# Optimization experiments

Measured on AMD Instinct MI355X. Metric: run time of the kernel, lower is better.

Reference implementation:

```python
import jax, jax.numpy as jnp
import numpy as np

H = 128  # hidden_dim
F = 256  # node_feature_dim
N = 40000      # layer-graph nodes
E = 640000     # layer-graph edges
L = 8          # number of head graphs
NH = 8192      # nodes per head graph
EH = 131072    # edges per head graph


def setup_inputs() -> dict:
    key = jax.random.key(0)
    ks = jax.random.split(key, 32)
    s = 0.05
    inp = {
        "x": jax.random.normal(ks[0], (N, F), jnp.float32),
        "edge_index": jax.random.randint(ks[1], (2, E), 0, N, jnp.int64) if jax.config.jax_enable_x64 else jax.random.randint(ks[1], (2, E), 0, N, jnp.int32),
        "head_x": jax.random.normal(ks[2], (L, NH, F), jnp.float32),
        "head_edge_index": jax.random.randint(ks[3], (L, 2, EH), 0, NH, jnp.int32),
        # feature encoder (Linear-ReLU-Linear-ReLU)
        "enc_w1": jax.random.normal(ks[4], (F, H), jnp.float32) * s, "enc_b1": jnp.zeros((H,), jnp.float32),
        "enc_w2": jax.random.normal(ks[5], (H, H), jnp.float32) * s, "enc_b2": jnp.zeros((H,), jnp.float32),
        # two GCNConv layers
        "gnn_w1": jax.random.normal(ks[6], (H, H), jnp.float32) * s, "gnn_b1": jnp.zeros((H,), jnp.float32),
        "gnn_w2": jax.random.normal(ks[7], (H, H), jnp.float32) * s, "gnn_b2": jnp.zeros((H,), jnp.float32),
        # layer policy head
        "lp_w1": jax.random.normal(ks[8], (H, H), jnp.float32) * s, "lp_b1": jnp.zeros((H,), jnp.float32),
        "lp_w2": jax.random.normal(ks[9], (H, 1), jnp.float32) * s, "lp_b2": jnp.zeros((1,), jnp.float32),
        # head policy head
        "hp_w1": jax.random.normal(ks[10], (H, H), jnp.float32) * s, "hp_b1": jnp.zeros((H,), jnp.float32),
        "hp_w2": jax.random.normal(ks[11], (H, 1), jnp.float32) * s, "hp_b2": jnp.zeros((1,), jnp.float32),
        # value net
        "v_w1": jax.random.normal(ks[12], (H, H), jnp.float32) * s, "v_b1": jnp.zeros((H,), jnp.float32),
        "v_w2": jax.random.normal(ks[13], (H, 1), jnp.float32) * s, "v_b2": jnp.zeros((1,), jnp.float32),
    }
    return inp


def _gcn(h, src, dst, w, b, n):
    # torch_geometric GCNConv: add self loops, symmetric normalization, then X@W + b
    h = h @ w
    loop = jnp.arange(n, dtype=src.dtype)
    si = jnp.concatenate([src, loop])
    di = jnp.concatenate([dst, loop])
    deg = jax.ops.segment_sum(jnp.ones_like(di, dtype=h.dtype), di, num_segments=n)
    dinv = jnp.where(deg > 0, jax.lax.rsqrt(deg), 0.0)
    msg = h[si] * (dinv[si] * dinv[di])[:, None]  # gather + per-edge scale
    return jax.ops.segment_sum(msg, di, num_segments=n) + b


def reference(x, edge_index, head_x, head_edge_index,
              enc_w1, enc_b1, enc_w2, enc_b2,
              gnn_w1, gnn_b1, gnn_w2, gnn_b2,
              lp_w1, lp_b1, lp_w2, lp_b2,
              hp_w1, hp_b1, hp_w2, hp_b2,
              v_w1, v_b1, v_w2, v_b2):
    relu = jax.nn.relu

    def encode(z):
        return relu(relu(z @ enc_w1 + enc_b1) @ enc_w2 + enc_b2)

    def gnn_stack(z, ei, n):
        z = encode(z)
        z = relu(_gcn(z, ei[0], ei[1], gnn_w1, gnn_b1, n))
        z = relu(_gcn(z, ei[0], ei[1], gnn_w2, gnn_b2, n))
        return z

    h = gnn_stack(x, edge_index, x.shape[0])                    # [N, H]
    layer_probs = jax.nn.sigmoid(relu(h @ lp_w1 + lp_b1) @ lp_w2 + lp_b2)[:, 0]  # [N]
    state_value = relu(h.mean(axis=0) @ v_w1 + v_b1) @ v_w2 + v_b2               # [1]

    def head_fn(hx, hei):
        hh = gnn_stack(hx, hei, hx.shape[0])
        return jax.nn.sigmoid(relu(hh @ hp_w1 + hp_b1) @ hp_w2 + hp_b2)[:, 0]
    head_probs = jax.vmap(head_fn)(head_x, head_edge_index)     # [L, NH]

    # original gates head computation on layer_probs[i] > 0.5 (data-dependent);
    # here we compute all head graphs and expose the gate mask explicitly.
    head_mask = layer_probs[:head_x.shape[0]] > 0.5
    return layer_probs, head_probs, head_mask, state_value
```

## Files before the change

### kernel.cpp

```cpp
#include <hip/hip_runtime.h>
#include <math.h>


typedef unsigned short ushort_t;
using short8 = __attribute__((ext_vector_type(8))) short;
using f32x4  = __attribute__((ext_vector_type(4))) float;

constexpr int N_L  = 40000;
constexpr int E_L  = 640000;
constexpr int L_H  = 8;
constexpr int N_H1 = 8192;
constexpr int E_H1 = 131072;
constexpr int N_HT = 65536;
constexpr int E_HT = 1048576;
constexpr int E_T  = E_L + E_HT;
constexpr int NLP  = 40064;
constexpr int R_T  = 105600;
constexpr int HBASE = 40064;

constexpr size_t OFF_SAF  = 0;
constexpr size_t OFF_HB   = (size_t)NLP * 512;
constexpr size_t OFF_ZPAD = OFF_HB + (size_t)N_HT * 256;
constexpr size_t OFF_SBH  = OFF_ZPAD + 512;
constexpr size_t OFF_SBL  = OFF_SBH + (size_t)R_T * 256;
constexpr size_t OFF_WTH  = OFF_SBL + (size_t)NLP * 256;
constexpr size_t OFF_WTL  = OFF_WTH + 229376;
constexpr size_t OFF_DINV = OFF_WTL + 229376;
constexpr size_t OFF_HSUM = OFF_DINV + (size_t)R_T * 4;
constexpr size_t OFF_DEG  = OFF_HSUM + 512;
constexpr size_t OFF_RP   = OFF_DEG + (size_t)R_T * 4;
constexpr size_t OFF_EG   = OFF_RP + (size_t)(R_T + 1) * 4;
constexpr size_t OFF_BSUM = OFF_EG + (size_t)(E_T + 16) * 4;

constexpr int ZIDX_L = (int)(OFF_ZPAD / 512);
constexpr int ZIDX_H = R_T;

static_assert(OFF_ZPAD % 512 == 0, "zpad alignment");


__device__ __forceinline__ unsigned short bf16_rne(float f) {
  unsigned u = __float_as_uint(f);
  unsigned r = u + 0x7FFFu + ((u >> 16) & 1u);
  return (unsigned short)(r >> 16);
}
__device__ __forceinline__ float bfhi_f(unsigned short h) {
  return __uint_as_float((unsigned)h << 16);
}
__device__ __forceinline__ void split2(float f, unsigned short& h, unsigned short& l) {
  h = bf16_rne(f);
  l = bf16_rne(f - bfhi_f(h));
}

__device__ __forceinline__ void gload16(const void* g, void* l) {
  __builtin_amdgcn_global_load_lds((__attribute__((address_space(1))) void*)(g),
                                   (__attribute__((address_space(3))) void*)(l),
                                   16, 0, 0);
}


__global__ __launch_bounds__(256) void count_deg_all(const int* __restrict__ ei,
                                                     const int* __restrict__ hei,
                                                     int* __restrict__ indeg,
                                                     int* __restrict__ rank) {
  int i = blockIdx.x * 256 + threadIdx.x;
  if (i < E_L) {
    rank[i] = atomicAdd(&indeg[ei[E_L + i]], 1);
  } else if (i < E_T) {
    int t = i - E_L;
    int l = t >> 17, e = t & (E_H1 - 1);
    rank[i] = atomicAdd(&indeg[HBASE + l * N_H1 + hei[l * 2 * E_H1 + E_H1 + e]], 1);
  }
}

__global__ __launch_bounds__(256) void dinv_kernel(const int* __restrict__ indeg,
                                                   float* __restrict__ dinv, int n) {
  int i = blockIdx.x * 256 + threadIdx.x;
  if (i < n) dinv[i] = 1.0f / sqrtf((float)(indeg[i] + 1));
}

__global__ __launch_bounds__(1024) void scan_block(const int* __restrict__ in, int n,
                                                   int* __restrict__ out,
                                                   int* __restrict__ bsum) {
  __shared__ int s[1024];
  int t = threadIdx.x;
  int i = blockIdx.x * 1024 + t;
  int v = (i < n) ? in[i] : 0;
  s[t] = v;
  __syncthreads();
  for (int off = 1; off < 1024; off <<= 1) {
    int x = (t >= off) ? s[t - off] : 0;
    __syncthreads();
    s[t] += x;
    __syncthreads();
  }
  if (i < n) out[i] = s[t] - v;
  if (t == 1023) bsum[blockIdx.x] = s[t];
}

__global__ __launch_bounds__(64) void scan_top128(int* __restrict__ bsum, int nb) {
  int lane = threadIdx.x;
  int a = (lane < nb) ? bsum[lane] : 0;
  int b = (lane + 64 < nb) ? bsum[lane + 64] : 0;
  int ia = a;
  for (int off = 1; off < 64; off <<= 1) {
    int x = __shfl_up(ia, off);
    if (lane >= off) ia += x;
  }
  int ta = __shfl(ia, 63);
  int ib = b;
  for (int off = 1; off < 64; off <<= 1) {
    int x = __shfl_up(ib, off);
    if (lane >= off) ib += x;
  }
  int tb = __shfl(ib, 63);
  if (lane < nb) bsum[lane] = ia - a;
  if (lane + 64 < nb) bsum[lane + 64] = ta + ib - b;
  if (lane == 0) bsum[nb] = ta + tb;
}

__global__ __launch_bounds__(256) void scan_fix(int* __restrict__ rowptr,
                                                const int* __restrict__ bsum,
                                                int n, int nb) {
  int i = blockIdx.x * 256 + threadIdx.x;
  if (i < n) {
    rowptr[i] += bsum[i >> 10];
  } else if (i == n) {
    rowptr[n] = bsum[nb];
  }
}

__global__ __launch_bounds__(256) void fill_csr_all(const int* __restrict__ ei,
                                                    const int* __restrict__ hei,
                                                    const int* __restrict__ rowptr,
                                                    const int* __restrict__ rank,
                                                    unsigned* __restrict__ eg) {
  int i = blockIdx.x * 256 + threadIdx.x;
  if (i < E_L) {
    int dst = ei[E_L + i];
    int src = ei[i];
    eg[rowptr[dst] + rank[i]] = (unsigned)src;
  } else if (i < E_T) {
    int t = i - E_L;
    int l = t >> 17, e = t & (E_H1 - 1);
    int b2 = l * 2 * E_H1;
    int dst = HBASE + l * N_H1 + hei[b2 + E_H1 + e];
    int src = HBASE + l * N_H1 + hei[b2 + e];
    eg[rowptr[dst] + rank[i]] = (unsigned)src;
  }
}


__global__ __launch_bounds__(256) void conv_weights(
    const float* __restrict__ w0, const float* __restrict__ w1,
    const float* __restrict__ w2, const float* __restrict__ w3,
    const float* __restrict__ w4, const float* __restrict__ w5,
    unsigned short* __restrict__ th, unsigned short* __restrict__ tl) {
  int t = blockIdx.x * 256 + threadIdx.x;
  const float* src; int K, dstoff, idx;
  if (t < 32768) { src = w0; K = 256; dstoff = 0; idx = t; }
  else {
    int s = (t - 32768) >> 14;
    idx = (t - 32768) & 16383;
    K = 128;
    dstoff = 32768 + s * 16384;
    src = s == 0 ? w1 : s == 1 ? w2 : s == 2 ? w3 : s == 3 ? w4 : w5;
  }
  int k = idx >> 7, c = idx & 127;
  unsigned short h_, l_;
  split2(src[idx], h_, l_);
  th[dstoff + c * K + k] = h_;
  tl[dstoff + c * K + k] = l_;
}


template <bool SPLIT>
__device__ __forceinline__ void stage_w_t(const unsigned short* Wth,
                                          const unsigned short* Wtl, int K, int kc,
                                          char* Ws_h, char* Ws_l,
                                          int wv, int rsub, int xr) {
#pragma unroll
  for (int j = 0; j < 4; ++j) {
    int q = wv * 4 + j;
    int c = q * 8 + rsub;
    size_t gb = ((size_t)c * K + kc) * 2 + (size_t)xr * 16;
    gload16((const char*)Wth + gb, Ws_h + q * 1024);
    if constexpr (SPLIT) gload16((const char*)Wtl + gb, Ws_l + q * 1024);
  }
}

template <bool SPLIT>
__device__ __forceinline__ void mfma_chunk_t(const char* As_h, const char* As_l,
                                             const char* Ws_h, const char* Ws_l,
                                             int wv, int g, int li,
                                             f32x4 acc[2][8]) {
  short8 fa_h[2][2], fa_l[2][2];
#pragma unroll
  for (int m = 0; m < 2; ++m)
#pragma unroll
    for (int ks = 0; ks < 2; ++ks) {
      int row = wv * 32 + m * 16 + li;
      int off = row * 128 + ks * 64 + g * 16;
      off ^= (row & 7) << 4;
      fa_h[m][ks] = *(const short8*)(As_h + off);
      if constexpr (SPLIT) fa_l[m][ks] = *(const short8*)(As_l + off);
    }
#pragma unroll
  for (int nh = 0; nh < 2; ++nh) {
    short8 fb_h[4][2], fb_l[4][2];
#pragma unroll
    for (int n = 0; n < 4; ++n)
#pragma unroll
      for (int ks = 0; ks < 2; ++ks) {
        int c = nh * 64 + n * 16 + li;
        int off = c * 128 + ks * 64 + g * 16;
        off ^= (c & 7) << 4;
        fb_h[n][ks] = *(const short8*)(Ws_h + off);
        if constexpr (SPLIT) fb_l[n][ks] = *(const short8*)(Ws_l + off);
      }
#pragma unroll
    for (int m = 0; m < 2; ++m)
#pragma unroll
      for (int n = 0; n < 4; ++n)
#pragma unroll
        for (int ks = 0; ks < 2; ++ks) {
          f32x4 a_ = acc[m][nh * 4 + n];
          a_ = __builtin_amdgcn_mfma_f32_16x16x32_bf16(fa_h[m][ks], fb_h[n][ks], a_, 0, 0, 0);
          if constexpr (SPLIT) {
            a_ = __builtin_amdgcn_mfma_f32_16x16x32_bf16(fa_h[m][ks], fb_l[n][ks], a_, 0, 0, 0);
            a_ = __builtin_amdgcn_mfma_f32_16x16x32_bf16(fa_l[m][ks], fb_h[n][ks], a_, 0, 0, 0);
          }
          acc[m][nh * 4 + n] = a_;
        }
  }
}

template <bool SPLIT>
__device__ __forceinline__ void write_h_slice_t(const f32x4 acc[2][8],
                                                const float* bj, int kc,
                                                char* As_h, char* As_l,
                                                int wv, int g, int li) {
#pragma unroll
  for (int m = 0; m < 2; ++m)
#pragma unroll
    for (int jj = 0; jj < 4; ++jj) {
      int j = (kc >> 4) + jj;
#pragma unroll
      for (int r = 0; r < 4; ++r) {
        float o = fmaxf(acc[m][j][r] + bj[j], 0.f);
        int row = wv * 32 + m * 16 + g * 4 + r;
        int cl = jj * 16 + li;
        int byte = row * 128 + ((((cl >> 3) ^ (row & 7)) << 4) | ((cl & 7) * 2));
        if constexpr (SPLIT) {
          unsigned short h_, l_;
          split2(o, h_, l_);
          *(unsigned short*)(As_h + byte) = h_;
          *(unsigned short*)(As_l + byte) = l_;
        } else {
          *(unsigned short*)(As_h + byte) = bf16_rne(o);
        }
      }
    }
}

__device__ __forceinline__ void write_g_out(const f32x4 acc[2][8],
                                            const float* __restrict__ dinvg,
                                            float* __restrict__ G,
                                            unsigned short* __restrict__ Hb,
                                            int row0, int wv, int g, int li) {
  if (row0 < NLP) {
#pragma unroll
    for (int m = 0; m < 2; ++m)
#pragma unroll
      for (int r = 0; r < 4; ++r) {
        int rowg = row0 + wv * 32 + m * 16 + g * 4 + r;
        float dvr = dinvg[rowg];
#pragma unroll
        for (int j = 0; j < 8; ++j)
          G[(size_t)rowg * 128 + j * 16 + li] = acc[m][j][r] * dvr;
      }
  } else {
#pragma unroll
    for (int m = 0; m < 2; ++m)
#pragma unroll
      for (int r = 0; r < 4; ++r) {
        int rowg = row0 + wv * 32 + m * 16 + g * 4 + r;
        float dvr = dinvg[rowg];
        int rl = rowg - HBASE;
#pragma unroll
        for (int j = 0; j < 8; ++j)
          Hb[(size_t)rl * 128 + j * 16 + li] = bf16_rne(acc[m][j][r] * dvr);
      }
  }
}


template <bool SPLIT>
__device__ __forceinline__ void enc_body(
    const float* __restrict__ xs, int lclamp,
    const unsigned short* __restrict__ W1h, const unsigned short* __restrict__ W1l,
    const unsigned short* __restrict__ W2h, const unsigned short* __restrict__ W2l,
    const unsigned short* __restrict__ Wgh, const unsigned short* __restrict__ Wgl,
    const float* __restrict__ b1, const float* __restrict__ b2,
    const float* __restrict__ dinvg,
    float* __restrict__ G, unsigned short* __restrict__ Hb,
    char* As_h, char* As_l, char* Ws_h, char* Ws_l,
    int tid, int wv, int g, int li, int row0, int lrow0, int rsub, int xr) {
  float bj1[8], bj2[8];
#pragma unroll
  for (int j = 0; j < 8; ++j) {
    bj1[j] = b1[j * 16 + li];
    bj2[j] = b2[j * 16 + li];
  }

  f32x4 acc1[2][8];
#pragma unroll
  for (int m = 0; m < 2; ++m)
#pragma unroll
    for (int j = 0; j < 8; ++j) acc1[m][j] = f32x4{0.f, 0.f, 0.f, 0.f};

#pragma unroll
  for (int kc = 0; kc < 256; kc += 64) {
    __syncthreads();
    stage_w_t<SPLIT>(W1h, W1l, 256, kc, Ws_h, Ws_l, wv, rsub, xr);
    {
      int r = tid >> 1, hf = tid & 1;
      int lrow = min(lrow0 + r, lclamp);
      const float* src = xs + (size_t)lrow * 256 + kc + hf * 32;
#pragma unroll
      for (int i = 0; i < 4; ++i) {
        float4 a = ((const float4*)src)[2 * i];
        float4 b = ((const float4*)src)[2 * i + 1];
        float f[8] = {a.x, a.y, a.z, a.w, b.x, b.y, b.z, b.w};
        short8 vh, vl;
#pragma unroll
        for (int e = 0; e < 8; ++e) {
          if constexpr (SPLIT) {
            unsigned short h_, l_;
            split2(f[e], h_, l_);
            vh[e] = (short)h_;
            vl[e] = (short)l_;
          } else {
            vh[e] = (short)bf16_rne(f[e]);
          }
        }
        int xu = hf * 4 + i;
        int u = r * 8 + (xu ^ (r & 7));
        *(short8*)(As_h + u * 16) = vh;
        if constexpr (SPLIT) *(short8*)(As_l + u * 16) = vl;
      }
    }
    __syncthreads();
    mfma_chunk_t<SPLIT>(As_h, As_l, Ws_h, Ws_l, wv, g, li, acc1);
  }

  f32x4 acc2[2][8];
#pragma unroll
  for (int m = 0; m < 2; ++m)
#pragma unroll
    for (int j = 0; j < 8; ++j) acc2[m][j] = f32x4{0.f, 0.f, 0.f, 0.f};

#pragma unroll
  for (int kc = 0; kc < 128; kc += 64) {
    __syncthreads();
    stage_w_t<SPLIT>(W2h, W2l, 128, kc, Ws_h, Ws_l, wv, rsub, xr);
    write_h_slice_t<SPLIT>(acc1, bj1, kc, As_h, As_l, wv, g, li);
    __syncthreads();
    mfma_chunk_t<SPLIT>(As_h, As_l, Ws_h, Ws_l, wv, g, li, acc2);
  }

  f32x4 acc3[2][8];
#pragma unroll
  for (int m = 0; m < 2; ++m)
#pragma unroll
    for (int j = 0; j < 8; ++j) acc3[m][j] = f32x4{0.f, 0.f, 0.f, 0.f};

#pragma unroll
  for (int kc = 0; kc < 128; kc += 64) {
    __syncthreads();
    stage_w_t<SPLIT>(Wgh, Wgl, 128, kc, Ws_h, Ws_l, wv, rsub, xr);
    write_h_slice_t<SPLIT>(acc2, bj2, kc, As_h, As_l, wv, g, li);
    __syncthreads();
    mfma_chunk_t<SPLIT>(As_h, As_l, Ws_h, Ws_l, wv, g, li, acc3);
  }

  write_g_out(acc3, dinvg, G, Hb, row0, wv, g, li);
}

__global__ __launch_bounds__(256, 2) void enc_fused(
    const float* __restrict__ x, const float* __restrict__ head_x,
    const unsigned short* __restrict__ W1h, const unsigned short* __restrict__ W1l,
    const unsigned short* __restrict__ W2h, const unsigned short* __restrict__ W2l,
    const unsigned short* __restrict__ Wgh, const unsigned short* __restrict__ Wgl,
    const float* __restrict__ b1, const float* __restrict__ b2,
    const float* __restrict__ dinvg,
    float* __restrict__ G, unsigned short* __restrict__ Hb) {
  __shared__ __align__(16) char lds[65536];
  char* As_h = lds;
  char* As_l = lds + 16384;
  char* Ws_h = lds + 32768;
  char* Ws_l = lds + 49152;

  const int tid = threadIdx.x;
  const int lane = tid & 63;
  const int wv = tid >> 6;
  const int g = lane >> 4;
  const int li = lane & 15;
  const int row0 = blockIdx.x * 128;
  const int rsub = lane >> 3;
  const int xr = (lane & 7) ^ ((lane >> 3) & 7);

  if (row0 < NLP) {
    enc_body<true>(x, N_L - 1, W1h, W1l, W2h, W2l, Wgh, Wgl, b1, b2, dinvg, G, Hb,
                   As_h, As_l, Ws_h, Ws_l, tid, wv, g, li, row0, row0, rsub, xr);
  } else {
    enc_body<false>(head_x, N_HT - 1, W1h, nullptr, W2h, nullptr, Wgh, nullptr,
                    b1, b2, dinvg, G, Hb,
                    As_h, As_l, Ws_h, Ws_l, tid, wv, g, li, row0, row0 - NLP,
                    rsub, xr);
  }
}


template <bool SPLIT>
__device__ __forceinline__ void mm_g_body(
    const unsigned short* __restrict__ Ah, const unsigned short* __restrict__ Al,
    const unsigned short* __restrict__ Wth, const unsigned short* __restrict__ Wtl,
    char* As_h, char* As_l, char* Ws_h, char* Ws_l,
    int wv, int g, int li, int row0, int rsub, int xr, f32x4 acc[2][8]) {
  constexpr int K = 128;
#pragma unroll
  for (int kc = 0; kc < K; kc += 64) {
    __syncthreads();
    stage_w_t<SPLIT>(Wth, Wtl, K, kc, Ws_h, Ws_l, wv, rsub, xr);
#pragma unroll
    for (int j = 0; j < 4; ++j) {
      int q = wv * 4 + j;
      int r = q * 8 + rsub;
      size_t gb = ((size_t)(row0 + r) * K + kc) * 2 + (size_t)xr * 16;
      gload16((const char*)Ah + gb, As_h + q * 1024);
      if constexpr (SPLIT) gload16((const char*)Al + gb, As_l + q * 1024);
    }
    __syncthreads();
    mfma_chunk_t<SPLIT>(As_h, As_l, Ws_h, Ws_l, wv, g, li, acc);
  }
}

__global__ __launch_bounds__(256) void mm_g(
    const unsigned short* __restrict__ Ah, const unsigned short* __restrict__ Al,
    const unsigned short* __restrict__ Wth, const unsigned short* __restrict__ Wtl,
    const float* __restrict__ dinvg,
    float* __restrict__ Cf, unsigned short* __restrict__ Hb) {
  __shared__ __align__(16) char lds[65536];
  char* As_h = lds;
  char* As_l = lds + 16384;
  char* Ws_h = lds + 32768;
  char* Ws_l = lds + 49152;

  const int tid = threadIdx.x;
  const int lane = tid & 63;
  const int wv = tid >> 6;
  const int g = lane >> 4;
  const int li = lane & 15;
  const int row0 = blockIdx.x * 128;
  const int rsub = lane >> 3;
  const int xr = (lane & 7) ^ ((lane >> 3) & 7);

  f32x4 acc[2][8];
#pragma unroll
  for (int m = 0; m < 2; ++m)
#pragma unroll
    for (int j = 0; j < 8; ++j) acc[m][j] = f32x4{0.f, 0.f, 0.f, 0.f};

  if (row0 < NLP)
    mm_g_body<true>(Ah, Al, Wth, Wtl, As_h, As_l, Ws_h, Ws_l,
                    wv, g, li, row0, rsub, xr, acc);
  else
    mm_g_body<false>(Ah, nullptr, Wth, nullptr, As_h, As_l, Ws_h, Ws_l,
                     wv, g, li, row0, rsub, xr, acc);

  write_g_out(acc, dinvg, Cf, Hb, row0, wv, g, li);
}


__global__ __launch_bounds__(256) void mm_policy(
    const unsigned short* __restrict__ Ah, const unsigned short* __restrict__ Al,
    const unsigned short* __restrict__ Wth_l, const unsigned short* __restrict__ Wtl_l,
    const unsigned short* __restrict__ Wth_h,
    const float* __restrict__ b1l, const float* __restrict__ b1h,
    const float* __restrict__ w2l, const float* __restrict__ w2h,
    const float* __restrict__ b2l, const float* __restrict__ b2h,
    float* __restrict__ out_l, float* __restrict__ out_h) {
  __shared__ __align__(16) char lds[65536];
  char* As_h = lds;
  char* As_l = lds + 16384;
  char* Ws_h = lds + 32768;
  char* Ws_l = lds + 49152;

  const int tid = threadIdx.x;
  const int lane = tid & 63;
  const int wv = tid >> 6;
  const int g = lane >> 4;
  const int li = lane & 15;
  const int row0 = blockIdx.x * 128;
  const bool isl = row0 < NLP;
  const int rsub = lane >> 3;
  const int xr = (lane & 7) ^ ((lane >> 3) & 7);

  const float* bias = isl ? b1l : b1h;
  const float* pw2  = isl ? w2l : w2h;
  const float* pb2  = isl ? b2l : b2h;

  f32x4 acc[2][8];
#pragma unroll
  for (int m = 0; m < 2; ++m)
#pragma unroll
    for (int j = 0; j < 8; ++j) acc[m][j] = f32x4{0.f, 0.f, 0.f, 0.f};

  if (isl)
    mm_g_body<true>(Ah, Al, Wth_l, Wtl_l, As_h, As_l, Ws_h, Ws_l,
                    wv, g, li, row0, rsub, xr, acc);
  else
    mm_g_body<false>(Ah, nullptr, Wth_h, nullptr, As_h, As_l, Ws_h, Ws_l,
                     wv, g, li, row0, rsub, xr, acc);

  float w2c[8], bj[8];
#pragma unroll
  for (int j = 0; j < 8; ++j) {
    w2c[j] = pw2[j * 16 + li];
    bj[j]  = bias[j * 16 + li];
  }
#pragma unroll
  for (int m = 0; m < 2; ++m)
#pragma unroll
    for (int r = 0; r < 4; ++r) {
      float p = 0.f;
#pragma unroll
      for (int j = 0; j < 8; ++j) {
        float o = fmaxf(acc[m][j][r] + bj[j], 0.f);
        p = fmaf(o, w2c[j], p);
      }
      p += __shfl_xor(p, 1);
      p += __shfl_xor(p, 2);
      p += __shfl_xor(p, 4);
      p += __shfl_xor(p, 8);
      if (li == 0) {
        int rowg = row0 + wv * 32 + m * 16 + g * 4 + r;
        if (isl) {
          if (rowg < N_L) out_l[rowg] = 1.0f / (1.0f + expf(-(p + pb2[0])));
        } else {
          out_h[rowg - HBASE] = 1.0f / (1.0f + expf(-(p + pb2[0])));
        }
      }
    }
}


__global__ __launch_bounds__(256) void agg_packed(const float* __restrict__ Hin,
                                                  const unsigned short* __restrict__ Hb,
                                                  const float* __restrict__ dinvg,
                                                  const int* __restrict__ rowptr,
                                                  const unsigned* __restrict__ eg,
                                                  const float* __restrict__ bias,
                                                  unsigned short* __restrict__ Oh,
                                                  unsigned short* __restrict__ Ol) {
  int b = blockIdx.x;
  {
    int x = b & 7, j = b >> 3;
    b = (j < 626) ? (x * 626 + j) : (5008 + x * 1024 + (j - 626));
  }
  const int lane = threadIdx.x & 63;
  const int wv = threadIdx.x >> 6;
  const int half = lane >> 5;
  const int hl = lane & 31;
  const int v = b * 8 + wv * 2 + half;

  const float4* H4 = (const float4*)Hin;
  const ushort4* Hb4 = (const ushort4*)Hb;

  float dv = dinvg[v];
  int e0 = rowptr[v], e1 = rowptr[v + 1];
  int deg = e1 - e0;

  float4 acc;
  if (v < NLP) {
    acc = H4[(size_t)v * 32 + hl];
  } else {
    ushort4 t = Hb4[(size_t)(v - HBASE) * 32 + hl];
    acc.x = bfhi_f(t.x);
    acc.y = bfhi_f(t.y);
    acc.z = bfhi_f(t.z);
    acc.w = bfhi_f(t.w);
  }

  int nb = (deg + 15) >> 4;
  int nbo = __shfl_xor(nb, 32);
  int nbmax = max(nb, nbo);

  if (v < NLP) {
    for (int t = 0; t < nbmax; ++t) {
      int e = t * 16;
      unsigned pr = 0;
      if (hl < 16 && e + hl < deg) pr = eg[e0 + e + hl];
      float4 xs[16];
#pragma unroll
      for (int i = 0; i < 16; ++i) {
        unsigned pe = (unsigned)__shfl((int)pr, (half << 5) | i);
        int u = (e + i < deg) ? (int)pe : ZIDX_L;
        xs[i] = H4[(size_t)u * 32 + hl];
      }
#pragma unroll
      for (int i = 0; i < 16; ++i) {
        acc.x += xs[i].x;
        acc.y += xs[i].y;
        acc.z += xs[i].z;
        acc.w += xs[i].w;
      }
    }
  } else {
    for (int t = 0; t < nbmax; ++t) {
      int e = t * 16;
      unsigned pr = 0;
      if (hl < 16 && e + hl < deg) pr = eg[e0 + e + hl];
      ushort4 xs[16];
#pragma unroll
      for (int i = 0; i < 16; ++i) {
        unsigned pe = (unsigned)__shfl((int)pr, (half << 5) | i);
        int u = (e + i < deg) ? (int)pe : ZIDX_H;
        xs[i] = Hb4[(size_t)(u - HBASE) * 32 + hl];
      }
#pragma unroll
      for (int i = 0; i < 16; ++i) {
        acc.x += bfhi_f(xs[i].x);
        acc.y += bfhi_f(xs[i].y);
        acc.z += bfhi_f(xs[i].z);
        acc.w += bfhi_f(xs[i].w);
      }
    }
  }

  float4 bb = ((const float4*)bias)[hl];
  acc.x = fmaxf(fmaf(dv, acc.x, bb.x), 0.f);
  acc.y = fmaxf(fmaf(dv, acc.y, bb.y), 0.f);
  acc.z = fmaxf(fmaf(dv, acc.z, bb.z), 0.f);
  acc.w = fmaxf(fmaf(dv, acc.w, bb.w), 0.f);

  if (v < NLP) {
    ushort4 th, tl;
    split2(acc.x, th.x, tl.x);
    split2(acc.y, th.y, tl.y);
    split2(acc.z, th.z, tl.z);
    split2(acc.w, th.w, tl.w);
    ((ushort4*)Oh)[(size_t)v * 32 + hl] = th;
    ((ushort4*)Ol)[(size_t)v * 32 + hl] = tl;
  } else {
    ushort4 th;
    th.x = bf16_rne(acc.x);
    th.y = bf16_rne(acc.y);
    th.z = bf16_rne(acc.z);
    th.w = bf16_rne(acc.w);
    ((ushort4*)Oh)[(size_t)v * 32 + hl] = th;
  }
}


__global__ __launch_bounds__(128) void colsum_split(const unsigned short* __restrict__ Hh,
                                                    const unsigned short* __restrict__ Hl,
                                                    float* __restrict__ hsum, int n) {
  int f = threadIdx.x;
  int r0 = blockIdx.x * 128;
  int r1 = min(r0 + 128, n);
  float acc = 0.f;
  for (int r = r0; r < r1; ++r) {
    size_t idx = (size_t)r * 128 + f;
    acc += bfhi_f(Hh[idx]) + bfhi_f(Hl[idx]);
  }
  atomicAdd(&hsum[f], acc);
}

__global__ __launch_bounds__(128) void value_kernel(const float* __restrict__ hsum,
                                                    const float* __restrict__ w1,
                                                    const float* __restrict__ b1,
                                                    const float* __restrict__ w2,
                                                    const float* __restrict__ b2,
                                                    float* __restrict__ out) {
  __shared__ float hm[128];
  __shared__ float red[128];
  int t = threadIdx.x;
  hm[t] = hsum[t] * (1.0f / (float)N_L);
  __syncthreads();
  float acc = b1[t];
  for (int k = 0; k < 128; ++k) acc = fmaf(hm[k], w1[k * 128 + t], acc);
  red[t] = fmaxf(acc, 0.f) * w2[t];
  for (int off = 64; off > 0; off >>= 1) {
    __syncthreads();
    if (t < off) red[t] += red[t + off];
  }
  __syncthreads();
  if (t == 0) out[0] = red[0] + b2[0];
}

__global__ __launch_bounds__(64) void mask_kernel(const float* __restrict__ lp,
                                                  float* __restrict__ out) {
  int i = threadIdx.x;
  if (i < L_H) out[i] = (lp[i] > 0.5f) ? 1.0f : 0.0f;
}


extern "C" void kernel_launch(void* const* d_in, const int* in_sizes, int n_in,
                              void* d_out, int out_size, void* d_ws, size_t ws_size,
                              hipStream_t stream) {
  const float* x      = (const float*)d_in[0];
  const int*   ei     = (const int*)d_in[1];
  const float* head_x = (const float*)d_in[2];
  const int*   hei    = (const int*)d_in[3];
  const float* enc_w1 = (const float*)d_in[4];
  const float* enc_b1 = (const float*)d_in[5];
  const float* enc_w2 = (const float*)d_in[6];
  const float* enc_b2 = (const float*)d_in[7];
  const float* gnn_w1 = (const float*)d_in[8];
  const float* gnn_b1 = (const float*)d_in[9];
  const float* gnn_w2 = (const float*)d_in[10];
  const float* gnn_b2 = (const float*)d_in[11];
  const float* lp_w1  = (const float*)d_in[12];
  const float* lp_b1  = (const float*)d_in[13];
  const float* lp_w2  = (const float*)d_in[14];
  const float* lp_b2  = (const float*)d_in[15];
  const float* hp_w1  = (const float*)d_in[16];
  const float* hp_b1  = (const float*)d_in[17];
  const float* hp_w2  = (const float*)d_in[18];
  const float* hp_b2  = (const float*)d_in[19];
  const float* v_w1   = (const float*)d_in[20];
  const float* v_b1   = (const float*)d_in[21];
  const float* v_w2   = (const float*)d_in[22];
  const float* v_b2   = (const float*)d_in[23];
  float* out = (float*)d_out;

  char* base = (char*)d_ws;
  float* SAf = (float*)(base + OFF_SAF);
  unsigned short* Hb = (unsigned short*)(base + OFF_HB);
  unsigned short* SBh = (unsigned short*)(base + OFF_SBH);
  unsigned short* SBl = (unsigned short*)(base + OFF_SBL);
  unsigned short* WTh = (unsigned short*)(base + OFF_WTH);
  unsigned short* WTl = (unsigned short*)(base + OFF_WTL);
  float* dinv_g = (float*)(base + OFF_DINV);
  float* hsum   = (float*)(base + OFF_HSUM);
  int* indeg_g  = (int*)(base + OFF_DEG);
  int* rowptr_g = (int*)(base + OFF_RP);
  unsigned* eg  = (unsigned*)(base + OFF_EG);
  int* bsum     = (int*)(base + OFF_BSUM);
  int* rank     = (int*)(base + OFF_SAF);

  const int WT_ENC1 = 0, WT_ENC2 = 32768, WT_G1 = 49152, WT_G2 = 65536,
            WT_LP = 81920, WT_HP = 98304;

  const int OUT_LP = 0, OUT_HP = N_L, OUT_MASK = N_L + N_HT, OUT_SV = N_L + N_HT + L_H;

  hipMemsetAsync(indeg_g, 0, (size_t)R_T * sizeof(int), stream);
  hipMemsetAsync(hsum, 0, 128 * sizeof(float), stream);
  hipMemsetAsync(base + OFF_ZPAD, 0, 512, stream);

  conv_weights<<<448, 256, 0, stream>>>(enc_w1, enc_w2, gnn_w1, gnn_w2, lp_w1, hp_w1,
                                        WTh, WTl);

  count_deg_all<<<(E_T + 255) / 256, 256, 0, stream>>>(ei, hei, indeg_g, rank);
  dinv_kernel<<<(R_T + 255) / 256, 256, 0, stream>>>(indeg_g, dinv_g, R_T);

  scan_block<<<(R_T + 1023) / 1024, 1024, 0, stream>>>(indeg_g, R_T, rowptr_g, bsum);
  scan_top128<<<1, 64, 0, stream>>>(bsum, (R_T + 1023) / 1024);
  scan_fix<<<(R_T + 256) / 256, 256, 0, stream>>>(rowptr_g, bsum, R_T,
                                                  (R_T + 1023) / 1024);
  fill_csr_all<<<(E_T + 255) / 256, 256, 0, stream>>>(ei, hei, rowptr_g, rank, eg);

  enc_fused<<<R_T / 128, 256, 0, stream>>>(
      x, head_x,
      WTh + WT_ENC1, WTl + WT_ENC1,
      WTh + WT_ENC2, WTl + WT_ENC2,
      WTh + WT_G1,   WTl + WT_G1,
      enc_b1, enc_b2, dinv_g, SAf, Hb);

  agg_packed<<<R_T / 8, 256, 0, stream>>>(SAf, Hb, dinv_g, rowptr_g, eg, gnn_b1,
                                          SBh, SBl);

  mm_g<<<R_T / 128, 256, 0, stream>>>(SBh, SBl, WTh + WT_G2, WTl + WT_G2,
                                      dinv_g, SAf, Hb);
  agg_packed<<<R_T / 8, 256, 0, stream>>>(SAf, Hb, dinv_g, rowptr_g, eg, gnn_b2,
                                          SBh, SBl);

  mm_policy<<<R_T / 128, 256, 0, stream>>>(
      SBh, SBl,
      WTh + WT_LP, WTl + WT_LP, WTh + WT_HP,
      lp_b1, hp_b1, lp_w2, hp_w2, lp_b2, hp_b2,
      out + OUT_LP, out + OUT_HP);

  colsum_split<<<(N_L + 127) / 128, 128, 0, stream>>>(SBh, SBl, hsum, N_L);
  value_kernel<<<1, 128, 0, stream>>>(hsum, v_w1, v_b1, v_w2, v_b2, out + OUT_SV);

  mask_kernel<<<1, 64, 0, stream>>>(out + OUT_LP, out + OUT_MASK);
}
```

Baseline: 390.8 us.

## Merge preprocessing kernels and overlap CSR fill with encoder blocks

Weight conversion and degree counting now run as one launch, dinv is computed inside scan_fix, and the CSR fill runs as extra blocks appended to the encoder kernel's grid. This removes three kernel launches and lets the scatter-heavy fill overlap with the matmul-heavy encoder. Rank storage moves to the SBH buffer because SAf is now written by the encoder while the fill blocks still read rank. The fill blocks still declare the 64KB LDS allocation, which may limit how many of them are resident alongside encoder blocks.

```diff
diff --git a/kernel.cpp b/kernel.cpp
--- a/kernel.cpp
+++ b/kernel.cpp
@@ -17,6 +17,10 @@
 constexpr int NLP  = 40064;
 constexpr int R_T  = 105600;
 constexpr int HBASE = 40064;
+
+constexpr int NB_ENC  = R_T / 128;
+constexpr int NB_FILL = (E_T + 255) / 256;
+constexpr int NB_CONV = 448;
 
 constexpr size_t OFF_SAF  = 0;
 constexpr size_t OFF_HB   = (size_t)NLP * 512;
@@ -58,25 +62,41 @@
 }
 
 
-__global__ __launch_bounds__(256) void count_deg_all(const int* __restrict__ ei,
-                                                     const int* __restrict__ hei,
-                                                     int* __restrict__ indeg,
-                                                     int* __restrict__ rank) {
-  int i = blockIdx.x * 256 + threadIdx.x;
-  if (i < E_L) {
-    rank[i] = atomicAdd(&indeg[ei[E_L + i]], 1);
-  } else if (i < E_T) {
-    int t = i - E_L;
-    int l = t >> 17, e = t & (E_H1 - 1);
-    rank[i] = atomicAdd(&indeg[HBASE + l * N_H1 + hei[l * 2 * E_H1 + E_H1 + e]], 1);
-  }
-}
-
-__global__ __launch_bounds__(256) void dinv_kernel(const int* __restrict__ indeg,
-                                                   float* __restrict__ dinv, int n) {
-  int i = blockIdx.x * 256 + threadIdx.x;
-  if (i < n) dinv[i] = 1.0f / sqrtf((float)(indeg[i] + 1));
-}
+__global__ __launch_bounds__(256) void prep_csr(
+    const float* __restrict__ w0, const float* __restrict__ w1,
+    const float* __restrict__ w2, const float* __restrict__ w3,
+    const float* __restrict__ w4, const float* __restrict__ w5,
+    unsigned short* __restrict__ th, unsigned short* __restrict__ tl,
+    const int* __restrict__ ei, const int* __restrict__ hei,
+    int* __restrict__ indeg, int* __restrict__ rank) {
+  if (blockIdx.x < NB_CONV) {
+    int t = blockIdx.x * 256 + threadIdx.x;
+    const float* src; int K, dstoff, idx;
+    if (t < 32768) { src = w0; K = 256; dstoff = 0; idx = t; }
+    else {
+      int s = (t - 32768) >> 14;
+      idx = (t - 32768) & 16383;
+      K = 128;
+      dstoff = 32768 + s * 16384;
+      src = s == 0 ? w1 : s == 1 ? w2 : s == 2 ? w3 : s == 3 ? w4 : w5;
+    }
+    int k = idx >> 7, c = idx & 127;
+    unsigned short h_, l_;
+    split2(src[idx], h_, l_);
+    th[dstoff + c * K + k] = h_;
+    tl[dstoff + c * K + k] = l_;
+  } else {
+    int i = (blockIdx.x - NB_CONV) * 256 + threadIdx.x;
+    if (i < E_L) {
+      rank[i] = atomicAdd(&indeg[ei[E_L + i]], 1);
+    } else if (i < E_T) {
+      int t = i - E_L;
+      int l = t >> 17, e = t & (E_H1 - 1);
+      rank[i] = atomicAdd(&indeg[HBASE + l * N_H1 + hei[l * 2 * E_H1 + E_H1 + e]], 1);
+    }
+  }
+}
+
 
 __global__ __launch_bounds__(1024) void scan_block(const int* __restrict__ in, int n,
                                                    int* __restrict__ out,
@@ -120,56 +140,16 @@
 
 __global__ __launch_bounds__(256) void scan_fix(int* __restrict__ rowptr,
                                                 const int* __restrict__ bsum,
+                                                const int* __restrict__ indeg,
+                                                float* __restrict__ dinv,
                                                 int n, int nb) {
   int i = blockIdx.x * 256 + threadIdx.x;
   if (i < n) {
     rowptr[i] += bsum[i >> 10];
+    dinv[i] = 1.0f / sqrtf((float)(indeg[i] + 1));
   } else if (i == n) {
     rowptr[n] = bsum[nb];
   }
-}
-
-__global__ __launch_bounds__(256) void fill_csr_all(const int* __restrict__ ei,
-                                                    const int* __restrict__ hei,
-                                                    const int* __restrict__ rowptr,
-                                                    const int* __restrict__ rank,
-                                                    unsigned* __restrict__ eg) {
-  int i = blockIdx.x * 256 + threadIdx.x;
-  if (i < E_L) {
-    int dst = ei[E_L + i];
-    int src = ei[i];
-    eg[rowptr[dst] + rank[i]] = (unsigned)src;
-  } else if (i < E_T) {
-    int t = i - E_L;
-    int l = t >> 17, e = t & (E_H1 - 1);
-    int b2 = l * 2 * E_H1;
-    int dst = HBASE + l * N_H1 + hei[b2 + E_H1 + e];
-    int src = HBASE + l * N_H1 + hei[b2 + e];
-    eg[rowptr[dst] + rank[i]] = (unsigned)src;
-  }
-}
-
-
-__global__ __launch_bounds__(256) void conv_weights(
-    const float* __restrict__ w0, const float* __restrict__ w1,
-    const float* __restrict__ w2, const float* __restrict__ w3,
-    const float* __restrict__ w4, const float* __restrict__ w5,
-    unsigned short* __restrict__ th, unsigned short* __restrict__ tl) {
-  int t = blockIdx.x * 256 + threadIdx.x;
-  const float* src; int K, dstoff, idx;
-  if (t < 32768) { src = w0; K = 256; dstoff = 0; idx = t; }
-  else {
-    int s = (t - 32768) >> 14;
-    idx = (t - 32768) & 16383;
-    K = 128;
-    dstoff = 32768 + s * 16384;
-    src = s == 0 ? w1 : s == 1 ? w2 : s == 2 ? w3 : s == 3 ? w4 : w5;
-  }
-  int k = idx >> 7, c = idx & 127;
-  unsigned short h_, l_;
-  split2(src[idx], h_, l_);
-  th[dstoff + c * K + k] = h_;
-  tl[dstoff + c * K + k] = l_;
 }
 
 
@@ -393,8 +373,29 @@
     const unsigned short* __restrict__ Wgh, const unsigned short* __restrict__ Wgl,
     const float* __restrict__ b1, const float* __restrict__ b2,
     const float* __restrict__ dinvg,
-    float* __restrict__ G, unsigned short* __restrict__ Hb) {
+    float* __restrict__ G, unsigned short* __restrict__ Hb,
+    const int* __restrict__ ei, const int* __restrict__ hei,
+    const int* __restrict__ rowptr, const int* __restrict__ rank,
+    unsigned* __restrict__ eg) {
   __shared__ __align__(16) char lds[65536];
+
+  if (blockIdx.x >= NB_ENC) {
+    int i = (blockIdx.x - NB_ENC) * 256 + threadIdx.x;
+    if (i < E_L) {
+      int dst = ei[E_L + i];
+      int src = ei[i];
+      eg[rowptr[dst] + rank[i]] = (unsigned)src;
+    } else if (i < E_T) {
+      int t = i - E_L;
+      int l = t >> 17, e = t & (E_H1 - 1);
+      int b2o = l * 2 * E_H1;
+      int dst = HBASE + l * N_H1 + hei[b2o + E_H1 + e];
+      int src = HBASE + l * N_H1 + hei[b2o + e];
+      eg[rowptr[dst] + rank[i]] = (unsigned)src;
+    }
+    return;
+  }
+
   char* As_h = lds;
   char* As_l = lds + 16384;
   char* Ws_h = lds + 32768;
@@ -748,7 +749,7 @@
   int* rowptr_g = (int*)(base + OFF_RP);
   unsigned* eg  = (unsigned*)(base + OFF_EG);
   int* bsum     = (int*)(base + OFF_BSUM);
-  int* rank     = (int*)(base + OFF_SAF);
+  int* rank     = (int*)(base + OFF_SBH);
 
   const int WT_ENC1 = 0, WT_ENC2 = 32768, WT_G1 = 49152, WT_G2 = 65536,
             WT_LP = 81920, WT_HP = 98304;
@@ -759,24 +760,22 @@
   hipMemsetAsync(hsum, 0, 128 * sizeof(float), stream);
   hipMemsetAsync(base + OFF_ZPAD, 0, 512, stream);
 
-  conv_weights<<<448, 256, 0, stream>>>(enc_w1, enc_w2, gnn_w1, gnn_w2, lp_w1, hp_w1,
-                                        WTh, WTl);
-
-  count_deg_all<<<(E_T + 255) / 256, 256, 0, stream>>>(ei, hei, indeg_g, rank);
-  dinv_kernel<<<(R_T + 255) / 256, 256, 0, stream>>>(indeg_g, dinv_g, R_T);
+  prep_csr<<<NB_CONV + NB_FILL, 256, 0, stream>>>(
+      enc_w1, enc_w2, gnn_w1, gnn_w2, lp_w1, hp_w1, WTh, WTl,
+      ei, hei, indeg_g, rank);
 
   scan_block<<<(R_T + 1023) / 1024, 1024, 0, stream>>>(indeg_g, R_T, rowptr_g, bsum);
   scan_top128<<<1, 64, 0, stream>>>(bsum, (R_T + 1023) / 1024);
-  scan_fix<<<(R_T + 256) / 256, 256, 0, stream>>>(rowptr_g, bsum, R_T,
-                                                  (R_T + 1023) / 1024);
-  fill_csr_all<<<(E_T + 255) / 256, 256, 0, stream>>>(ei, hei, rowptr_g, rank, eg);
-
-  enc_fused<<<R_T / 128, 256, 0, stream>>>(
+  scan_fix<<<(R_T + 256) / 256, 256, 0, stream>>>(rowptr_g, bsum, indeg_g, dinv_g,
+                                                  R_T, (R_T + 1023) / 1024);
+
+  enc_fused<<<NB_ENC + NB_FILL, 256, 0, stream>>>(
       x, head_x,
       WTh + WT_ENC1, WTl + WT_ENC1,
       WTh + WT_ENC2, WTl + WT_ENC2,
       WTh + WT_G1,   WTl + WT_G1,
-      enc_b1, enc_b2, dinv_g, SAf, Hb);
+      enc_b1, enc_b2, dinv_g, SAf, Hb,
+      ei, hei, rowptr_g, rank, eg);
 
   agg_packed<<<R_T / 8, 256, 0, stream>>>(SAf, Hb, dinv_g, rowptr_g, eg, gnn_b1,
                                           SBh, SBl);
```

Result: faster. 381.1 us (-2.5%).
